# Optimization experiments

Measured on AMD Instinct MI355X. Metric: run time of the kernel, lower is better.

The kernel has to match this reference:

```python
import jax, jax.numpy as jnp
import numpy as np

N_HEADS = 16
D_IN = 1024
D_K = 64          # per-head
D_V_HEAD = 1024 // N_HEADS  # 64 per-head


def setup_inputs() -> dict:
    key = jax.random.key(0)
    k1, k2, k3, k4, k5 = jax.random.split(key, 5)
    B, LQ, LK = 2, 2048, 2048
    s = 1.0 / np.sqrt(D_IN)
    return {
        "input_q": jax.random.normal(k1, (B, LQ, D_IN), dtype=jnp.float32),
        "input_k": jax.random.normal(k2, (B, LK, D_IN), dtype=jnp.float32),
        # nn.Linear weights stored as [out, in]; we use [in, out] for x @ W
        "wq": jax.random.uniform(k3, (D_IN, D_K * N_HEADS), jnp.float32, -s, s),
        "wk": jax.random.uniform(k4, (D_IN, D_K * N_HEADS), jnp.float32, -s, s),
        "wv": jax.random.uniform(k5, (D_IN, D_V_HEAD * N_HEADS), jnp.float32, -s, s),
    }


def reference(input_q, input_k, wq, wk, wv):
    B, LQ, _ = input_q.shape
    _, LK, _ = input_k.shape
    # project and split heads: [B, H, L, d]
    q = (input_q @ wq).reshape(B, LQ, N_HEADS, D_K).transpose(0, 2, 1, 3)
    k = (input_k @ wk).reshape(B, LK, N_HEADS, D_K).transpose(0, 2, 1, 3)
    v = (input_k @ wv).reshape(B, LK, N_HEADS, D_V_HEAD).transpose(0, 2, 1, 3)
    attn = jnp.einsum("bhqd,bhkd->bhqk", q, k) / jnp.sqrt(jnp.float32(D_K))
    attn = jax.nn.softmax(attn, axis=-1)
    out = jnp.einsum("bhqk,bhkd->bhqd", attn, v)
    return out.transpose(0, 2, 1, 3).reshape(B, LQ, D_V_HEAD * N_HEADS)
```

## Files before the change

kernel.cpp:

```cpp
#include <hip/hip_runtime.h>

#define DIN 1024
#define LSEQ 2048

typedef _Float16 f16;
typedef _Float16 half8 __attribute__((ext_vector_type(8)));
typedef float floatx4 __attribute__((ext_vector_type(4)));

__device__ __forceinline__ void async_ld16(const void* g, void* l) {
  __builtin_amdgcn_global_load_lds(
      (const __attribute__((address_space(1))) void*)g,
      (__attribute__((address_space(3))) void*)l, 16, 0, 0);
}

__device__ __forceinline__ float fast_exp2(float x) {
#if __has_builtin(__builtin_amdgcn_exp2f)
  return __builtin_amdgcn_exp2f(x);
#else
  return exp2f(x);
#endif
}

__device__ __forceinline__ unsigned int pack2_f16(float a, float b) {
#if __has_builtin(__builtin_amdgcn_cvt_pkrtz)
  typedef __fp16 fp16x2 __attribute__((ext_vector_type(2)));
  fp16x2 h = __builtin_amdgcn_cvt_pkrtz(a, b);
  return __builtin_bit_cast(unsigned int, h);
#else
  union { f16 h[2]; unsigned int u; } pk;
  pk.h[0] = (f16)a; pk.h[1] = (f16)b;
  return pk.u;
#endif
}

__global__ void __launch_bounds__(256) kprep(const float* __restrict__ xq,
                                             const float* __restrict__ xk,
                                             const float* __restrict__ wq,
                                             const float* __restrict__ wk,
                                             const float* __restrict__ wv,
                                             f16* __restrict__ wqt,
                                             f16* __restrict__ wkt,
                                             f16* __restrict__ wvt,
                                             f16* __restrict__ xqh,
                                             f16* __restrict__ xkh) {
  int z = blockIdx.z;
  int tid = threadIdx.x;
  if (z < 3) {
    __shared__ float t[32][33];
    const float* src = z == 0 ? wq : (z == 1 ? wk : wv);
    f16* dst = z == 0 ? wqt : (z == 1 ? wkt : wvt);
    int k0 = blockIdx.x * 32, n0 = blockIdx.y * 32;
    int tx = tid & 31, ty = tid >> 5;
#pragma unroll
    for (int r = 0; r < 4; ++r)
      t[ty + r * 8][tx] = src[(k0 + ty + r * 8) * DIN + n0 + tx];
    __syncthreads();
#pragma unroll
    for (int r = 0; r < 4; ++r)
      dst[(n0 + ty + r * 8) * DIN + k0 + tx] = (f16)t[tx][ty + r * 8];
  } else {
    const float4* src = (const float4*)(z == 4 ? xk : xq);
    uint2* dst = (uint2*)(z == 4 ? xkh : xqh);
    int bx = blockIdx.y * 32 + blockIdx.x;
    int i = bx * 256 + tid;
#pragma unroll
    for (int it = 0; it < 4; ++it, i += 262144) {
      float4 v = src[i];
      union { unsigned int u[2]; uint2 w; } pk;
      pk.u[0] = pack2_f16(v.x, v.y);
      pk.u[1] = pack2_f16(v.z, v.w);
      dst[i] = pk.w;
    }
  }
}

template <int AMODE>
__global__ void __launch_bounds__(256) kproj(const float* __restrict__ xq,
                                             const float* __restrict__ xk,
                                             const f16* __restrict__ xqh,
                                             const f16* __restrict__ xkh,
                                             const f16* __restrict__ wqt,
                                             const f16* __restrict__ wkt,
                                             const f16* __restrict__ wvt,
                                             f16* __restrict__ qb,
                                             f16* __restrict__ kb,
                                             f16* __restrict__ vtb) {
  __shared__ __align__(16) char smem[34816];
  char* As = smem;
  char* Bs = smem + 16384;
  const float* X;
  const f16* Xh;
  const f16* W;
  int z = blockIdx.z;
  if (z == 0) { X = xq; Xh = xqh; W = wqt; }
  else if (z == 1) { X = xk; Xh = xkh; W = wkt; }
  else { X = xk; Xh = xkh; W = wvt; }
  float oscale = (z == 0) ? 0.18033688011112042f : 1.0f;
  int m0 = blockIdx.y * 128, n0 = blockIdx.x * 128;
  int tid = threadIdx.x, lane = tid & 63, wid = tid >> 6;
  int wm = wid >> 1, wn = wid & 1;
  int c15 = lane & 15, g = lane >> 4;
  int l8 = lane >> 3, l7 = lane & 7;
  int kk = 8 * (l7 ^ l8);
  int swz = (c15 & 7) << 4;
  floatx4 acc[4][4] = {};

  for (int kt = 0; kt < 16; ++kt) {
    int k0 = kt * 64;
    if constexpr (AMODE == 1) {
#pragma unroll
      for (int cc = 0; cc < 4; ++cc) {
        int c = wid * 4 + cc;
        async_ld16(&Xh[(m0 + c * 8 + l8) * DIN + k0 + kk], As + c * 1024);
        async_ld16(&W[(n0 + c * 8 + l8) * DIN + k0 + kk], Bs + c * 1024);
      }
    } else {
#pragma unroll
      for (int cc = 0; cc < 4; ++cc) {
        int c = wid * 4 + cc;
        async_ld16(&W[(n0 + c * 8 + l8) * DIN + k0 + kk], Bs + c * 1024);
      }
      int q = tid & 15;
#pragma unroll
      for (int p = 0; p < 8; ++p) {
        int row = p * 16 + (tid >> 4);
        const float4 v = *(const float4*)&X[(m0 + row) * DIN + k0 + q * 4];
        union { unsigned int u[2]; uint2 v2; } pk;
        pk.u[0] = pack2_f16(v.x, v.y);
        pk.u[1] = pack2_f16(v.z, v.w);
        *(uint2*)(As + row * 128 + ((q * 8) ^ ((row & 7) << 4))) = pk.v2;
      }
    }
    __syncthreads();
#pragma unroll
    for (int ks = 0; ks < 2; ++ks) {
      int koff = (ks * 64 + g * 16) ^ swz;
      half8 af[4], bf[4];
#pragma unroll
      for (int i = 0; i < 4; ++i)
        af[i] = *(const half8*)(As + (wm * 64 + i * 16 + c15) * 128 + koff);
#pragma unroll
      for (int j = 0; j < 4; ++j)
        bf[j] = *(const half8*)(Bs + (wn * 64 + j * 16 + c15) * 128 + koff);
#pragma unroll
      for (int i = 0; i < 4; ++i)
#pragma unroll
        for (int j = 0; j < 4; ++j)
          acc[i][j] = __builtin_amdgcn_mfma_f32_16x16x32_f16(af[i], bf[j], acc[i][j], 0, 0, 0);
    }
    __syncthreads();
  }

  if (z != 2) {
    f16* dst = (z == 0) ? qb : kb;
#pragma unroll
    for (int i = 0; i < 4; ++i) {
      int mrow = m0 + wm * 64 + i * 16 + 4 * g;
#pragma unroll
      for (int j = 0; j < 4; ++j) {
        int n = n0 + wn * 64 + j * 16 + c15;
        int h = n >> 6, d = n & 63;
#pragma unroll
        for (int r = 0; r < 4; ++r) {
          int m = mrow + r;
          int b = m >> 11, lrow = m & 2047;
          dst[(((b << 4) + h) * 2048 + lrow) * 64 + d] = (f16)(acc[i][j][r] * oscale);
        }
      }
    }
  } else {
#pragma unroll
    for (int i = 0; i < 4; ++i) {
      int mb = (wm * 64 + i * 16 + 4 * g) * 2;
#pragma unroll
      for (int j = 0; j < 4; ++j) {
        int nl = wn * 64 + j * 16 + c15;
        union { unsigned int u[2]; uint2 v; } pk;
        pk.u[0] = pack2_f16(acc[i][j][0], acc[i][j][1]);
        pk.u[1] = pack2_f16(acc[i][j][2], acc[i][j][3]);
        *(uint2*)(smem + nl * 272 + mb) = pk.v;
      }
    }
    __syncthreads();
    int rowp = tid >> 1, halfp = tid & 1;
    int n = n0 + rowp, h = n >> 6, d = n & 63;
    int b = m0 >> 11, lbase = m0 & 2047;
    f16* dstp = vtb + (((size_t)b * 16 + h) * 64 + d) * 2048 + lbase + halfp * 64;
    const char* srcl = smem + rowp * 272 + halfp * 128;
#pragma unroll
    for (int u = 0; u < 8; ++u)
      *(uint4*)(dstp + u * 8) = *(const uint4*)(srcl + u * 16);
  }
}

__global__ void __launch_bounds__(256, 4) kattn(const f16* __restrict__ qb,
                                                const f16* __restrict__ kbuf,
                                                const f16* __restrict__ vt,
                                                float* __restrict__ out) {
  __shared__ __align__(16) char smem[40960];
  char* Qs = smem + 32768;
  float* Ot = (float*)smem;

  int id = blockIdx.x;
  int wi = id >> 3;
  int bh = ((id & 7) << 2) | (wi >> 5);
  int q0 = (wi & 31) << 6;

  int tid = threadIdx.x, lane = tid & 63, w = tid >> 6;
  int c15 = lane & 15, g = lane >> 4;
  int l8 = lane >> 3, l7 = lane & 7;
  int kk = 8 * (l7 ^ l8);
  int swz = (c15 & 7) << 4;

  const f16* kbase = kbuf + (size_t)bh * 2048 * 64;
  const f16* vbase = vt + (size_t)bh * 64 * 2048;

  auto stageK = [&](int kv0) {
#pragma unroll
    for (int cc = 0; cc < 4; ++cc) {
      int c = w * 4 + cc;
      async_ld16(&kbase[(kv0 + c * 8 + l8) * 64 + kk], smem + c * 1024);
    }
  };
  auto stageV = [&](int kv0) {
#pragma unroll
    for (int cc = 0; cc < 4; ++cc) {
      int c = w * 4 + cc;
      int hb = c >> 3;
      int dv = (c & 7) * 8 + l8;
      async_ld16(&vbase[(size_t)dv * 2048 + kv0 + 64 * hb + kk],
                 smem + 16384 + c * 1024);
    }
  };

#pragma unroll
  for (int cc = 0; cc < 2; ++cc) {
    int c = w * 2 + cc;
    async_ld16(&qb[((size_t)bh * 2048 + q0 + c * 8 + l8) * 64 + kk],
               Qs + c * 1024);
  }
  stageK(0);
  stageV(0);
  __syncthreads();
  half8 qf[2];
#pragma unroll
  for (int ks = 0; ks < 2; ++ks)
    qf[ks] = *(const half8*)(Qs + (w * 16 + c15) * 128 + ((ks * 64 + g * 16) ^ swz));
  __syncthreads();

  float lsum = 0.f;
  floatx4 oacc[4] = {};
  char* Pw = smem + 32768 + w * 2048 + c15 * 128;
  int psw = swz;

  for (int t = 0; t < 16; ++t) {
    floatx4 st[8] = {};
    __builtin_amdgcn_s_setprio(1);
#pragma unroll
    for (int hb = 0; hb < 2; ++hb) {
      const char* Ks = smem + hb * 8192;
#pragma unroll
      for (int ks = 0; ks < 2; ++ks) {
        int koff = (ks * 64 + g * 16) ^ swz;
#pragma unroll
        for (int i = 0; i < 4; ++i) {
          half8 kf = *(const half8*)(Ks + (i * 16 + c15) * 128 + koff);
          st[hb * 4 + i] =
              __builtin_amdgcn_mfma_f32_16x16x32_f16(kf, qf[ks], st[hb * 4 + i], 0, 0, 0);
        }
      }
    }
    __builtin_amdgcn_s_setprio(0);
    __syncthreads();
    if (t < 15) stageK((t + 1) * 128);

    float ps0 = 0.f, ps1 = 0.f;
    unsigned int pu[16];
#pragma unroll
    for (int x = 0; x < 16; ++x) {
      float p0 = fast_exp2(st[x >> 1][(x & 1) * 2]);
      float p1 = fast_exp2(st[x >> 1][(x & 1) * 2 + 1]);
      ps0 += p0;
      ps1 += p1;
      pu[x] = pack2_f16(p0, p1);
    }
    lsum += ps0 + ps1;

    __builtin_amdgcn_s_setprio(1);
#pragma unroll
    for (int hb = 0; hb < 2; ++hb) {
#pragma unroll
      for (int ii = 0; ii < 4; ++ii) {
        union { unsigned int u[2]; uint2 v; } pk;
        pk.u[0] = pu[hb * 8 + 2 * ii];
        pk.u[1] = pu[hb * 8 + 2 * ii + 1];
        *(uint2*)(Pw + ((32 * ii + 8 * g) ^ psw)) = pk.v;
      }
      const char* Vs = smem + 16384 + hb * 8192;
#pragma unroll
      for (int kb = 0; kb < 2; ++kb) {
        half8 pf = *(const half8*)(Pw + ((kb * 64 + 16 * g) ^ psw));
        int koff = (kb * 64 + g * 16) ^ swz;
#pragma unroll
        for (int df = 0; df < 4; ++df) {
          half8 vf = *(const half8*)(Vs + (df * 16 + c15) * 128 + koff);
          oacc[df] = __builtin_amdgcn_mfma_f32_16x16x32_f16(vf, pf, oacc[df], 0, 0, 0);
        }
      }
    }
    __builtin_amdgcn_s_setprio(0);
    __syncthreads();
    if (t < 15) stageV((t + 1) * 128);
  }

  lsum += __shfl_xor(lsum, 16, 64);
  lsum += __shfl_xor(lsum, 32, 64);
  float inv = 1.f / lsum;

#pragma unroll
  for (int df = 0; df < 4; ++df) {
    floatx4 v = oacc[df] * inv;
    *(floatx4*)&Ot[(w * 16 + c15) * 68 + df * 16 + 4 * g] = v;
  }
  __syncthreads();
  int b = bh >> 4, h = bh & 15;
  int row = tid >> 2, seg = tid & 3;
  float* dstp = &out[((size_t)b * 2048 + q0 + row) * 1024 + h * 64 + seg * 16];
  const float* srcl = &Ot[row * 68 + seg * 16];
#pragma unroll
  for (int u = 0; u < 4; ++u)
    *(float4*)(dstp + u * 4) = *(const float4*)(srcl + u * 4);
}

extern "C" void kernel_launch(void* const* d_in, const int* in_sizes, int n_in,
                              void* d_out, int out_size, void* d_ws, size_t ws_size,
                              hipStream_t stream) {
  const float* xq = (const float*)d_in[0];
  const float* xk = (const float*)d_in[1];
  const float* wq = (const float*)d_in[2];
  const float* wk = (const float*)d_in[3];
  const float* wv = (const float*)d_in[4];
  char* ws = (char*)d_ws;
  f16* wqt = (f16*)(ws + (0ull << 20));
  f16* wkt = (f16*)(ws + (2ull << 20));
  f16* wvt = (f16*)(ws + (4ull << 20));

  bool fit = ws_size >= (46ull << 20);
  f16 *xqh, *xkh, *qbuf, *kbuf, *vtb;
  if (fit) {
    xqh  = (f16*)(ws + (6ull << 20));
    xkh  = (f16*)(ws + (14ull << 20));
    qbuf = (f16*)(ws + (22ull << 20));
    kbuf = (f16*)(ws + (30ull << 20));
    vtb  = (f16*)(ws + (38ull << 20));
  } else {
    xqh = xkh = nullptr;
    qbuf = (f16*)(ws + (6ull << 20));
    kbuf = (f16*)(ws + (14ull << 20));
    vtb  = (f16*)(ws + (22ull << 20));
  }

  kprep<<<dim3(32, 32, fit ? 5 : 3), 256, 0, stream>>>(xq, xk, wq, wk, wv,
                                                       wqt, wkt, wvt, xqh, xkh);
  if (fit) {
    kproj<1><<<dim3(8, 32, 3), 256, 0, stream>>>(xq, xk, xqh, xkh, wqt, wkt,
                                                 wvt, qbuf, kbuf, vtb);
  } else {
    kproj<0><<<dim3(8, 32, 3), 256, 0, stream>>>(xq, xk, xqh, xkh, wqt, wkt,
                                                 wvt, qbuf, kbuf, vtb);
  }
  kattn<<<1024, 256, 0, stream>>>(qbuf, kbuf, vtb, (float*)d_out);
}
```

Baseline: 104.6 us.

## Process two query tiles per wave in attention to reuse K/V fragments

Each wave now computes 32 query rows instead of 16, so every block covers 128 queries and the grid is halved. Each K and V fragment read from LDS feeds two MFMAs, which cuts LDS traffic and global K/V staging per query. Row normalization moves into the store epilogue, with the row sums passed through a small LDS buffer. In exchange, register and LDS use per block go up, the launch bound drops to 2 blocks per CU, and there are fewer, larger blocks to hide latency.

Result: faster. 102.3 us (median of 3 runs) (-2.2%).

```diff
diff --git a/kernel.cpp b/kernel.cpp
--- a/kernel.cpp
+++ b/kernel.cpp
@@ -193,18 +193,19 @@
   }
 }
 
-__global__ void __launch_bounds__(256, 4) kattn(const f16* __restrict__ qb,
+__global__ void __launch_bounds__(256, 2) kattn(const f16* __restrict__ qb,
                                                 const f16* __restrict__ kbuf,
                                                 const f16* __restrict__ vt,
                                                 float* __restrict__ out) {
-  __shared__ __align__(16) char smem[40960];
+  __shared__ __align__(16) char smem[49152];
   char* Qs = smem + 32768;
   float* Ot = (float*)smem;
+  float* lsb = (float*)(smem + 34816);
 
   int id = blockIdx.x;
   int wi = id >> 3;
-  int bh = ((id & 7) << 2) | (wi >> 5);
-  int q0 = (wi & 31) << 6;
+  int bh = ((id & 7) << 2) | (wi >> 4);
+  int q0 = (wi & 15) << 7;
 
   int tid = threadIdx.x, lane = tid & 63, w = tid >> 6;
   int c15 = lane & 15, g = lane >> 4;
@@ -234,27 +235,31 @@
   };
 
 #pragma unroll
-  for (int cc = 0; cc < 2; ++cc) {
-    int c = w * 2 + cc;
+  for (int cc = 0; cc < 4; ++cc) {
+    int c = w * 4 + cc;
     async_ld16(&qb[((size_t)bh * 2048 + q0 + c * 8 + l8) * 64 + kk],
                Qs + c * 1024);
   }
   stageK(0);
   stageV(0);
   __syncthreads();
-  half8 qf[2];
-#pragma unroll
-  for (int ks = 0; ks < 2; ++ks)
-    qf[ks] = *(const half8*)(Qs + (w * 16 + c15) * 128 + ((ks * 64 + g * 16) ^ swz));
+  half8 qf[2][2];
+#pragma unroll
+  for (int s = 0; s < 2; ++s)
+#pragma unroll
+    for (int ks = 0; ks < 2; ++ks)
+      qf[s][ks] = *(const half8*)(Qs + (w * 32 + s * 16 + c15) * 128 +
+                                  ((ks * 64 + g * 16) ^ swz));
   __syncthreads();
 
-  float lsum = 0.f;
-  floatx4 oacc[4] = {};
-  char* Pw = smem + 32768 + w * 2048 + c15 * 128;
+  float ls0 = 0.f, ls1 = 0.f;
+  floatx4 oacc[2][4] = {};
+  char* Pw0 = smem + 32768 + (w * 2 + 0) * 2048 + c15 * 128;
+  char* Pw1 = smem + 32768 + (w * 2 + 1) * 2048 + c15 * 128;
   int psw = swz;
 
   for (int t = 0; t < 16; ++t) {
-    floatx4 st[8] = {};
+    floatx4 st[2][8] = {};
     __builtin_amdgcn_s_setprio(1);
 #pragma unroll
     for (int hb = 0; hb < 2; ++hb) {
@@ -265,8 +270,10 @@
 #pragma unroll
         for (int i = 0; i < 4; ++i) {
           half8 kf = *(const half8*)(Ks + (i * 16 + c15) * 128 + koff);
-          st[hb * 4 + i] =
-              __builtin_amdgcn_mfma_f32_16x16x32_f16(kf, qf[ks], st[hb * 4 + i], 0, 0, 0);
+          st[0][hb * 4 + i] = __builtin_amdgcn_mfma_f32_16x16x32_f16(
+              kf, qf[0][ks], st[0][hb * 4 + i], 0, 0, 0);
+          st[1][hb * 4 + i] = __builtin_amdgcn_mfma_f32_16x16x32_f16(
+              kf, qf[1][ks], st[1][hb * 4 + i], 0, 0, 0);
         }
       }
     }
@@ -274,17 +281,31 @@
     __syncthreads();
     if (t < 15) stageK((t + 1) * 128);
 
-    float ps0 = 0.f, ps1 = 0.f;
-    unsigned int pu[16];
-#pragma unroll
-    for (int x = 0; x < 16; ++x) {
-      float p0 = fast_exp2(st[x >> 1][(x & 1) * 2]);
-      float p1 = fast_exp2(st[x >> 1][(x & 1) * 2 + 1]);
-      ps0 += p0;
-      ps1 += p1;
-      pu[x] = pack2_f16(p0, p1);
-    }
-    lsum += ps0 + ps1;
+    unsigned int pu0[16], pu1[16];
+    {
+      float ps0 = 0.f, ps1 = 0.f;
+#pragma unroll
+      for (int x = 0; x < 16; ++x) {
+        float p0 = fast_exp2(st[0][x >> 1][(x & 1) * 2]);
+        float p1 = fast_exp2(st[0][x >> 1][(x & 1) * 2 + 1]);
+        ps0 += p0;
+        ps1 += p1;
+        pu0[x] = pack2_f16(p0, p1);
+      }
+      ls0 += ps0 + ps1;
+    }
+    {
+      float ps0 = 0.f, ps1 = 0.f;
+#pragma unroll
+      for (int x = 0; x < 16; ++x) {
+        float p0 = fast_exp2(st[1][x >> 1][(x & 1) * 2]);
+        float p1 = fast_exp2(st[1][x >> 1][(x & 1) * 2 + 1]);
+        ps0 += p0;
+        ps1 += p1;
+        pu1[x] = pack2_f16(p0, p1);
+      }
+      ls1 += ps0 + ps1;
+    }
 
     __builtin_amdgcn_s_setprio(1);
 #pragma unroll
@@ -292,19 +313,24 @@
 #pragma unroll
       for (int ii = 0; ii < 4; ++ii) {
         union { unsigned int u[2]; uint2 v; } pk;
-        pk.u[0] = pu[hb * 8 + 2 * ii];
-        pk.u[1] = pu[hb * 8 + 2 * ii + 1];
-        *(uint2*)(Pw + ((32 * ii + 8 * g) ^ psw)) = pk.v;
+        pk.u[0] = pu0[hb * 8 + 2 * ii];
+        pk.u[1] = pu0[hb * 8 + 2 * ii + 1];
+        *(uint2*)(Pw0 + ((32 * ii + 8 * g) ^ psw)) = pk.v;
+        pk.u[0] = pu1[hb * 8 + 2 * ii];
+        pk.u[1] = pu1[hb * 8 + 2 * ii + 1];
+        *(uint2*)(Pw1 + ((32 * ii + 8 * g) ^ psw)) = pk.v;
       }
       const char* Vs = smem + 16384 + hb * 8192;
 #pragma unroll
       for (int kb = 0; kb < 2; ++kb) {
-        half8 pf = *(const half8*)(Pw + ((kb * 64 + 16 * g) ^ psw));
+        half8 pf0 = *(const half8*)(Pw0 + ((kb * 64 + 16 * g) ^ psw));
+        half8 pf1 = *(const half8*)(Pw1 + ((kb * 64 + 16 * g) ^ psw));
         int koff = (kb * 64 + g * 16) ^ swz;
 #pragma unroll
         for (int df = 0; df < 4; ++df) {
           half8 vf = *(const half8*)(Vs + (df * 16 + c15) * 128 + koff);
-          oacc[df] = __builtin_amdgcn_mfma_f32_16x16x32_f16(vf, pf, oacc[df], 0, 0, 0);
+          oacc[0][df] = __builtin_amdgcn_mfma_f32_16x16x32_f16(vf, pf0, oacc[0][df], 0, 0, 0);
+          oacc[1][df] = __builtin_amdgcn_mfma_f32_16x16x32_f16(vf, pf1, oacc[1][df], 0, 0, 0);
         }
       }
     }
@@ -313,23 +339,33 @@
     if (t < 15) stageV((t + 1) * 128);
   }
 
-  lsum += __shfl_xor(lsum, 16, 64);
-  lsum += __shfl_xor(lsum, 32, 64);
-  float inv = 1.f / lsum;
-
-#pragma unroll
-  for (int df = 0; df < 4; ++df) {
-    floatx4 v = oacc[df] * inv;
-    *(floatx4*)&Ot[(w * 16 + c15) * 68 + df * 16 + 4 * g] = v;
-  }
+  ls0 += __shfl_xor(ls0, 16, 64);
+  ls0 += __shfl_xor(ls0, 32, 64);
+  ls1 += __shfl_xor(ls1, 16, 64);
+  ls1 += __shfl_xor(ls1, 32, 64);
+  if (g == 0) {
+    lsb[w * 32 + c15] = ls0;
+    lsb[w * 32 + 16 + c15] = ls1;
+  }
+
+#pragma unroll
+  for (int s = 0; s < 2; ++s)
+#pragma unroll
+    for (int df = 0; df < 4; ++df)
+      *(floatx4*)&Ot[(w * 32 + s * 16 + c15) * 68 + df * 16 + 4 * g] =
+          oacc[s][df];
   __syncthreads();
+
   int b = bh >> 4, h = bh & 15;
-  int row = tid >> 2, seg = tid & 3;
-  float* dstp = &out[((size_t)b * 2048 + q0 + row) * 1024 + h * 64 + seg * 16];
-  const float* srcl = &Ot[row * 68 + seg * 16];
-#pragma unroll
-  for (int u = 0; u < 4; ++u)
-    *(float4*)(dstp + u * 4) = *(const float4*)(srcl + u * 4);
+  int row = tid >> 1, seg = tid & 1;
+  float inv = 1.f / lsb[row];
+  float* dstp = &out[((size_t)b * 2048 + q0 + row) * 1024 + h * 64 + seg * 32];
+  const float* srcl = &Ot[row * 68 + seg * 32];
+#pragma unroll
+  for (int u = 0; u < 8; ++u) {
+    floatx4 v = *(const floatx4*)(srcl + u * 4) * inv;
+    *(floatx4*)(dstp + u * 4) = v;
+  }
 }
 
 extern "C" void kernel_launch(void* const* d_in, const int* in_sizes, int n_in,
@@ -369,5 +405,5 @@
     kproj<0><<<dim3(8, 32, 3), 256, 0, stream>>>(xq, xk, xqh, xkh, wqt, wkt,
                                                  wvt, qbuf, kbuf, vtb);
   }
-  kattn<<<1024, 256, 0, stream>>>(qbuf, kbuf, vtb, (float*)d_out);
-}
+  kattn<<<512, 256, 0, stream>>>(qbuf, kbuf, vtb, (float*)d_out);
+}
```
